# Performance work log

Hardware: AMD Instinct MI355X
Metric: run time of the kernel (lower is better)

## Reference

```python
import jax, jax.numpy as jnp
import numpy as np

S, X, G = 2048, 2048, 2
INPUT_SIZE = (3, 32, 32)
F = int(np.prod(INPUT_SIZE))


def setup_inputs() -> dict:
    key = jax.random.key(0)
    k1, k2, k3 = jax.random.split(key, 3)
    samples = jax.random.normal(k1, (S,) + INPUT_SIZE, dtype=jnp.float32)
    x = jax.random.normal(k2, (X,) + INPUT_SIZE, dtype=jnp.float32)
    # per-feature std per gradation, kept in [0.1, 1.0) like ranges_std scaling
    std = jax.random.uniform(k3, (G, F), dtype=jnp.float32, minval=0.1, maxval=1.0)
    return {"samples": samples, "x": x, "std": std}


def reference(samples, x, std):
    # samples: [S, C, H, W], x: [X, C, H, W], std: [G, F]
    G_, F_ = std.shape
    s = samples.reshape(samples.shape[0], F_)  # [S, F]
    xf = x.reshape(x.shape[0], F_)             # [X, F]
    w = 1.0 / (std * std)                       # [G, F] precision
    # per-gradation normalizer: -0.5*F*log(2pi) - sum_f log(std)
    const = -0.5 * F_ * jnp.log(2.0 * jnp.pi) - jnp.sum(jnp.log(std), axis=1)  # [G]
    # sum_f -0.5*((s-x)/std)^2 expanded: -0.5*(s^2 w - 2 s w x + x^2 w)
    A = jnp.einsum('sf,gf->gs', s * s, w)        # [G, S]
    C = jnp.einsum('xf,gf->gx', xf * xf, w)      # [G, X]
    B = jnp.einsum('sf,gf,xf->gsx', s, w, xf)    # [G, S, X] cross term
    logits = -0.5 * (A[:, :, None] - 2.0 * B + C[:, None, :]) + const[:, None, None]
    lp = jax.nn.logsumexp(logits, axis=2)        # over x (mixture components)
    lp = jax.nn.logsumexp(lp, axis=0)            # over gradations
    return lp - jnp.log(jnp.float32(x.shape[0] * G_))
```

## Files before the change

kernel.cpp:

```cpp
#include <hip/hip_runtime.h>
#include <math.h>

#define S_N 2048
#define X_N 2048
#define G_N 2
#define F_N 3072

#define TM 128
#define TN 128
#define BK 64
#define ITERS (F_N / BK)

typedef __bf16 bf16;
typedef __bf16 bf16x4 __attribute__((ext_vector_type(4)));
typedef __bf16 bf16x8 __attribute__((ext_vector_type(8)));
typedef float f32x4 __attribute__((ext_vector_type(4)));
typedef int i32x4 __attribute__((ext_vector_type(4)));

#define LGKM_BARRIER() asm volatile("s_waitcnt lgkmcnt(0)\n\ts_barrier" ::: "memory")

__global__ void k_const(const float* __restrict__ stdv, float* __restrict__ constg,
                        float* __restrict__ rinv) {
  int g = blockIdx.x;
  int t = threadIdx.x;
  float s = 0.f;
  for (int f = t; f < F_N; f += 256) {
    float v = stdv[g * F_N + f];
    rinv[g * F_N + f] = 1.0f / v;
    s += logf(v);
  }
  for (int o = 32; o; o >>= 1) s += __shfl_xor(s, o);
  __shared__ float red[4];
  int w = t >> 6, l = t & 63;
  if (l == 0) red[w] = s;
  __syncthreads();
  if (t == 0) {
    float tot = red[0] + red[1] + red[2] + red[3];
    constg[g] = -0.5f * (float)F_N * 1.8378770664093453f - tot;
  }
}

__global__ void k_prep(const float* __restrict__ samples, const float* __restrict__ xin,
                       const float* __restrict__ rinv,
                       bf16* __restrict__ U, bf16* __restrict__ V,
                       float* __restrict__ A, float* __restrict__ C) {
  int r = blockIdx.x;
  int t = threadIdx.x;
  bool isS = (r < S_N);
  const float* src = isS ? (samples + (size_t)r * F_N) : (xin + (size_t)(r - S_N) * F_N);
  float4 row[3];
#pragma unroll
  for (int j = 0; j < 3; ++j) row[j] = ((const float4*)src)[t + j * 256];

  __shared__ float red[4];
  int w = t >> 6, l = t & 63;

  for (int g = 0; g < G_N; ++g) {
    const float4* sd = (const float4*)(rinv + (size_t)g * F_N);
    bf16* dst = isS ? (U + ((size_t)g * S_N + r) * F_N)
                    : (V + ((size_t)g * X_N + (r - S_N)) * F_N);
    float acc = 0.f;
#pragma unroll
    for (int j = 0; j < 3; ++j) {
      float4 d = sd[t + j * 256];
      float u0 = row[j].x * d.x;
      float u1 = row[j].y * d.y;
      float u2 = row[j].z * d.z;
      float u3 = row[j].w * d.w;
      bf16x4 b;
      b[0] = (bf16)u0; b[1] = (bf16)u1; b[2] = (bf16)u2; b[3] = (bf16)u3;
      float f0 = (float)b[0], f1 = (float)b[1], f2 = (float)b[2], f3 = (float)b[3];
      acc += f0 * f0 + f1 * f1 + f2 * f2 + f3 * f3;
      ((bf16x4*)dst)[t + j * 256] = b;
    }
    for (int o = 32; o; o >>= 1) acc += __shfl_xor(acc, o);
    __syncthreads();
    if (l == 0) red[w] = acc;
    __syncthreads();
    if (t == 0) {
      float tot = red[0] + red[1] + red[2] + red[3];
      if (isS) A[(size_t)g * S_N + r] = tot;
      else     C[(size_t)g * X_N + (r - S_N)] = tot;
    }
  }
}

__global__ __launch_bounds__(256, 2) void k_gemm(const bf16* __restrict__ U, const bf16* __restrict__ V,
                                                 const float* __restrict__ A, const float* __restrict__ C,
                                                 float* __restrict__ logits) {
  __shared__ i32x4 ldsA[2][TM * BK / 8];
  __shared__ i32x4 ldsB[2][TN * BK / 8];

  int t = threadIdx.x;
  int g = blockIdx.z;
  int bm = blockIdx.y * TM;
  int bn = blockIdx.x * TN;

  const bf16* Ub = U + ((size_t)g * S_N + bm) * F_N;
  const bf16* Vb = V + ((size_t)g * X_N + bn) * F_N;

  int wave = t >> 6, lane = t & 63;
  int wm = wave & 1, wn = wave >> 1;
  int r = lane & 15, q = lane >> 4;
  int fr = (r >> 1) & 7;
  int ck0 = q ^ fr;
  int ck1 = (4 | q) ^ fr;

  int row0 = t >> 3;
  int gcc = (t & 7) ^ ((t >> 4) & 7);
  const bf16* gA[4];
  const bf16* gB[4];
#pragma unroll
  for (int j = 0; j < 4; ++j) {
    gA[j] = Ub + (size_t)(row0 + j * 32) * F_N + gcc * 8;
    gB[j] = Vb + (size_t)(row0 + j * 32) * F_N + gcc * 8;
  }

  f32x4 acc[4][4] = {};
  int abase = (wm * 64 + r) * 8;
  int bbase = (wn * 64 + r) * 8;

  i32x4 sA0[4], sB0[4], sA1[4], sB1[4];

#pragma unroll
  for (int j = 0; j < 4; ++j) {
    sA0[j] = *(const i32x4*)(gA[j]);
    sB0[j] = *(const i32x4*)(gB[j]);
  }
#pragma unroll
  for (int j = 0; j < 4; ++j) {
    sA1[j] = *(const i32x4*)(gA[j] + BK);
    sB1[j] = *(const i32x4*)(gB[j] + BK);
  }
#pragma unroll
  for (int j = 0; j < 4; ++j) {
    ldsA[0][t + j * 256] = sA0[j];
    ldsB[0][t + j * 256] = sB0[j];
  }
  LGKM_BARRIER();

  for (int it = 0; it < ITERS; it += 2) {
    {
      int k2 = it + 2;
      int pk = (k2 < ITERS ? k2 : 0) * BK;
#pragma unroll
      for (int j = 0; j < 4; ++j) {
        sA0[j] = *(const i32x4*)(gA[j] + pk);
        sB0[j] = *(const i32x4*)(gB[j] + pk);
      }
#pragma unroll
      for (int ks = 0; ks < 2; ++ks) {
        int ck = ks ? ck1 : ck0;
        bf16x8 af[4], bfr[4];
#pragma unroll
        for (int mi = 0; mi < 4; ++mi)
          af[mi] = __builtin_bit_cast(bf16x8, ldsA[0][abase + mi * 128 + ck]);
#pragma unroll
        for (int ni = 0; ni < 4; ++ni)
          bfr[ni] = __builtin_bit_cast(bf16x8, ldsB[0][bbase + ni * 128 + ck]);
#pragma unroll
        for (int mi = 0; mi < 4; ++mi)
#pragma unroll
          for (int ni = 0; ni < 4; ++ni)
            acc[mi][ni] = __builtin_amdgcn_mfma_f32_16x16x32_bf16(af[mi], bfr[ni], acc[mi][ni], 0, 0, 0);
      }
#pragma unroll
      for (int j = 0; j < 4; ++j) {
        ldsA[1][t + j * 256] = sA1[j];
        ldsB[1][t + j * 256] = sB1[j];
      }
      LGKM_BARRIER();
    }
    {
      int k3 = it + 3;
      int pk = (k3 < ITERS ? k3 : 0) * BK;
#pragma unroll
      for (int j = 0; j < 4; ++j) {
        sA1[j] = *(const i32x4*)(gA[j] + pk);
        sB1[j] = *(const i32x4*)(gB[j] + pk);
      }
#pragma unroll
      for (int ks = 0; ks < 2; ++ks) {
        int ck = ks ? ck1 : ck0;
        bf16x8 af[4], bfr[4];
#pragma unroll
        for (int mi = 0; mi < 4; ++mi)
          af[mi] = __builtin_bit_cast(bf16x8, ldsA[1][abase + mi * 128 + ck]);
#pragma unroll
        for (int ni = 0; ni < 4; ++ni)
          bfr[ni] = __builtin_bit_cast(bf16x8, ldsB[1][bbase + ni * 128 + ck]);
#pragma unroll
        for (int mi = 0; mi < 4; ++mi)
#pragma unroll
          for (int ni = 0; ni < 4; ++ni)
            acc[mi][ni] = __builtin_amdgcn_mfma_f32_16x16x32_bf16(af[mi], bfr[ni], acc[mi][ni], 0, 0, 0);
      }
#pragma unroll
      for (int j = 0; j < 4; ++j) {
        ldsA[0][t + j * 256] = sA0[j];
        ldsB[0][t + j * 256] = sB0[j];
      }
      LGKM_BARRIER();
    }
  }

  const float* Ap = A + (size_t)g * S_N + bm + wm * 64;
  const float* Cp = C + (size_t)g * X_N + bn + wn * 64;
  float cv[4];
#pragma unroll
  for (int ni = 0; ni < 4; ++ni) cv[ni] = Cp[ni * 16 + r];
#pragma unroll
  for (int mi = 0; mi < 4; ++mi) {
#pragma unroll
    for (int i = 0; i < 4; ++i) {
      int rowl = wm * 64 + mi * 16 + q * 4 + i;
      float av = Ap[mi * 16 + q * 4 + i];
      float* orow = logits + ((size_t)g * S_N + bm + rowl) * X_N + bn + wn * 64;
#pragma unroll
      for (int ni = 0; ni < 4; ++ni)
        orow[ni * 16 + r] = acc[mi][ni][i] - 0.5f * (av + cv[ni]);
    }
  }
}

__global__ void k_lse(const float* __restrict__ logits, const float* __restrict__ constg,
                      float* __restrict__ out) {
  int s = blockIdx.x, t = threadIdx.x;
  float c0 = constg[0], c1 = constg[1];
  const float4* p0 = (const float4*)(logits + (size_t)s * X_N);
  const float4* p1 = (const float4*)(logits + ((size_t)S_N + s) * X_N);
  float4 v[4];
  v[0] = p0[t]; v[1] = p0[t + 256];
  v[2] = p1[t]; v[3] = p1[t + 256];
  v[0].x += c0; v[0].y += c0; v[0].z += c0; v[0].w += c0;
  v[1].x += c0; v[1].y += c0; v[1].z += c0; v[1].w += c0;
  v[2].x += c1; v[2].y += c1; v[2].z += c1; v[2].w += c1;
  v[3].x += c1; v[3].y += c1; v[3].z += c1; v[3].w += c1;

  float m = v[0].x;
#pragma unroll
  for (int j = 0; j < 4; ++j) {
    m = fmaxf(m, v[j].x); m = fmaxf(m, v[j].y);
    m = fmaxf(m, v[j].z); m = fmaxf(m, v[j].w);
  }
  for (int o = 32; o; o >>= 1) m = fmaxf(m, __shfl_xor(m, o));
  __shared__ float redm[4];
  __shared__ float reds[4];
  int w = t >> 6, l = t & 63;
  if (l == 0) redm[w] = m;
  __syncthreads();
  m = fmaxf(fmaxf(redm[0], redm[1]), fmaxf(redm[2], redm[3]));

  float sum = 0.f;
#pragma unroll
  for (int j = 0; j < 4; ++j) {
    sum += expf(v[j].x - m) + expf(v[j].y - m) + expf(v[j].z - m) + expf(v[j].w - m);
  }
  for (int o = 32; o; o >>= 1) sum += __shfl_xor(sum, o);
  if (l == 0) reds[w] = sum;
  __syncthreads();
  if (t == 0) {
    float tot = reds[0] + reds[1] + reds[2] + reds[3];
    out[s] = m + logf(tot) - 8.317766166719343f;
  }
}

extern "C" void kernel_launch(void* const* d_in, const int* in_sizes, int n_in,
                              void* d_out, int out_size, void* d_ws, size_t ws_size,
                              hipStream_t stream) {
  const float* samples = (const float*)d_in[0];
  const float* xin     = (const float*)d_in[1];
  const float* stdv    = (const float*)d_in[2];
  float* out = (float*)d_out;

  char* ws = (char*)d_ws;
  size_t off = 0;
  bf16* U = (bf16*)(ws + off);        off += (size_t)G_N * S_N * F_N * 2;
  bf16* V = (bf16*)(ws + off);        off += (size_t)G_N * X_N * F_N * 2;
  float* logits = (float*)(ws + off); off += (size_t)G_N * S_N * X_N * 4;
  float* A = (float*)(ws + off);      off += (size_t)G_N * S_N * 4;
  float* C = (float*)(ws + off);      off += (size_t)G_N * X_N * 4;
  float* constg = (float*)(ws + off); off += 256;
  float* rinv = (float*)(ws + off);   off += (size_t)G_N * F_N * 4;

  k_const<<<dim3(G_N), dim3(256), 0, stream>>>(stdv, constg, rinv);
  k_prep<<<dim3(S_N + X_N), dim3(256), 0, stream>>>(samples, xin, rinv, U, V, A, C);
  k_gemm<<<dim3(X_N / TN, S_N / TM, G_N), dim3(256), 0, stream>>>(U, V, A, C, logits);
  k_lse<<<dim3(S_N), dim3(256), 0, stream>>>(logits, constg, out);
}
```

Measured before the change: 162.2 us.

## Restructure GEMM with direct global-to-LDS loads, triple buffering, and 256x128 tiles

The bf16 GEMM now loads tiles straight from global memory into LDS with global_load_lds, so the data no longer passes through registers. It also uses a three-stage LDS ring with split-phase prefetch and per-phase barriers. The block grows to 512 threads covering a 256x128 output tile. Each iteration is split into two MFMA phases with setprio and sched_barrier so loads and math interleave. This targets register pressure and global-load latency, at the cost of more LDS per block and more barriers per iteration.

```diff
diff --git a/kernel.cpp b/kernel.cpp
--- a/kernel.cpp
+++ b/kernel.cpp
@@ -1,15 +1,17 @@
 #include <hip/hip_runtime.h>
 #include <math.h>
+#include <stdint.h>
 
 #define S_N 2048
 #define X_N 2048
 #define G_N 2
 #define F_N 3072
 
-#define TM 128
+#define TM 256
 #define TN 128
 #define BK 64
 #define ITERS (F_N / BK)
+#define NBUF 3
 
 typedef __bf16 bf16;
 typedef __bf16 bf16x4 __attribute__((ext_vector_type(4)));
@@ -17,7 +19,11 @@
 typedef float f32x4 __attribute__((ext_vector_type(4)));
 typedef int i32x4 __attribute__((ext_vector_type(4)));
 
-#define LGKM_BARRIER() asm volatile("s_waitcnt lgkmcnt(0)\n\ts_barrier" ::: "memory")
+__device__ __forceinline__ void gload_lds16(const bf16* g, void* l) {
+  __builtin_amdgcn_global_load_lds(
+      (const __attribute__((address_space(1))) void*)g,
+      (__attribute__((address_space(3))) void*)l, 16, 0, 0);
+}
 
 __global__ void k_const(const float* __restrict__ stdv, float* __restrict__ constg,
                         float* __restrict__ rinv) {
@@ -85,11 +91,11 @@
   }
 }
 
-__global__ __launch_bounds__(256, 2) void k_gemm(const bf16* __restrict__ U, const bf16* __restrict__ V,
+__global__ __launch_bounds__(512, 2) void k_gemm(const bf16* __restrict__ U, const bf16* __restrict__ V,
                                                  const float* __restrict__ A, const float* __restrict__ C,
                                                  float* __restrict__ logits) {
-  __shared__ i32x4 ldsA[2][TM * BK / 8];
-  __shared__ i32x4 ldsB[2][TN * BK / 8];
+  __shared__ i32x4 ldsA[NBUF][TM * BK / 8];
+  __shared__ i32x4 ldsB[NBUF][TN * BK / 8];
 
   int t = threadIdx.x;
   int g = blockIdx.z;
@@ -100,108 +106,97 @@
   const bf16* Vb = V + ((size_t)g * X_N + bn) * F_N;
 
   int wave = t >> 6, lane = t & 63;
-  int wm = wave & 1, wn = wave >> 1;
+  int wm = wave & 3, wn = wave >> 2;
   int r = lane & 15, q = lane >> 4;
   int fr = (r >> 1) & 7;
   int ck0 = q ^ fr;
   int ck1 = (4 | q) ^ fr;
+  int abase = (wm * 64 + r) * 8;
+  int bbase = (wn * 64 + r) * 8;
 
   int row0 = t >> 3;
   int gcc = (t & 7) ^ ((t >> 4) & 7);
   const bf16* gA[4];
-  const bf16* gB[4];
-#pragma unroll
-  for (int j = 0; j < 4; ++j) {
-    gA[j] = Ub + (size_t)(row0 + j * 32) * F_N + gcc * 8;
-    gB[j] = Vb + (size_t)(row0 + j * 32) * F_N + gcc * 8;
-  }
+  const bf16* gB[2];
+#pragma unroll
+  for (int j = 0; j < 4; ++j) gA[j] = Ub + (size_t)(row0 + j * 64) * F_N + gcc * 8;
+#pragma unroll
+  for (int j = 0; j < 2; ++j) gB[j] = Vb + (size_t)(row0 + j * 64) * F_N + gcc * 8;
 
   f32x4 acc[4][4] = {};
-  int abase = (wm * 64 + r) * 8;
-  int bbase = (wn * 64 + r) * 8;
-
-  i32x4 sA0[4], sB0[4], sA1[4], sB1[4];
-
-#pragma unroll
-  for (int j = 0; j < 4; ++j) {
-    sA0[j] = *(const i32x4*)(gA[j]);
-    sB0[j] = *(const i32x4*)(gB[j]);
-  }
-#pragma unroll
-  for (int j = 0; j < 4; ++j) {
-    sA1[j] = *(const i32x4*)(gA[j] + BK);
-    sB1[j] = *(const i32x4*)(gB[j] + BK);
-  }
-#pragma unroll
-  for (int j = 0; j < 4; ++j) {
-    ldsA[0][t + j * 256] = sA0[j];
-    ldsB[0][t + j * 256] = sB0[j];
-  }
-  LGKM_BARRIER();
-
-  for (int it = 0; it < ITERS; it += 2) {
-    {
-      int k2 = it + 2;
-      int pk = (k2 < ITERS ? k2 : 0) * BK;
-#pragma unroll
-      for (int j = 0; j < 4; ++j) {
-        sA0[j] = *(const i32x4*)(gA[j] + pk);
-        sB0[j] = *(const i32x4*)(gB[j] + pk);
-      }
-#pragma unroll
-      for (int ks = 0; ks < 2; ++ks) {
-        int ck = ks ? ck1 : ck0;
-        bf16x8 af[4], bfr[4];
-#pragma unroll
-        for (int mi = 0; mi < 4; ++mi)
-          af[mi] = __builtin_bit_cast(bf16x8, ldsA[0][abase + mi * 128 + ck]);
-#pragma unroll
-        for (int ni = 0; ni < 4; ++ni)
-          bfr[ni] = __builtin_bit_cast(bf16x8, ldsB[0][bbase + ni * 128 + ck]);
-#pragma unroll
-        for (int mi = 0; mi < 4; ++mi)
-#pragma unroll
-          for (int ni = 0; ni < 4; ++ni)
-            acc[mi][ni] = __builtin_amdgcn_mfma_f32_16x16x32_bf16(af[mi], bfr[ni], acc[mi][ni], 0, 0, 0);
-      }
-#pragma unroll
-      for (int j = 0; j < 4; ++j) {
-        ldsA[1][t + j * 256] = sA1[j];
-        ldsB[1][t + j * 256] = sB1[j];
-      }
-      LGKM_BARRIER();
-    }
-    {
-      int k3 = it + 3;
-      int pk = (k3 < ITERS ? k3 : 0) * BK;
-#pragma unroll
-      for (int j = 0; j < 4; ++j) {
-        sA1[j] = *(const i32x4*)(gA[j] + pk);
-        sB1[j] = *(const i32x4*)(gB[j] + pk);
-      }
-#pragma unroll
-      for (int ks = 0; ks < 2; ++ks) {
-        int ck = ks ? ck1 : ck0;
-        bf16x8 af[4], bfr[4];
-#pragma unroll
-        for (int mi = 0; mi < 4; ++mi)
-          af[mi] = __builtin_bit_cast(bf16x8, ldsA[1][abase + mi * 128 + ck]);
-#pragma unroll
-        for (int ni = 0; ni < 4; ++ni)
-          bfr[ni] = __builtin_bit_cast(bf16x8, ldsB[1][bbase + ni * 128 + ck]);
-#pragma unroll
-        for (int mi = 0; mi < 4; ++mi)
-#pragma unroll
-          for (int ni = 0; ni < 4; ++ni)
-            acc[mi][ni] = __builtin_amdgcn_mfma_f32_16x16x32_bf16(af[mi], bfr[ni], acc[mi][ni], 0, 0, 0);
-      }
-#pragma unroll
-      for (int j = 0; j < 4; ++j) {
-        ldsA[0][t + j * 256] = sA0[j];
-        ldsB[0][t + j * 256] = sB0[j];
-      }
-      LGKM_BARRIER();
-    }
+
+#pragma unroll
+  for (int j = 0; j < 4; ++j) gload_lds16(gA[j], &ldsA[0][t + j * 512]);
+#pragma unroll
+  for (int j = 0; j < 2; ++j) gload_lds16(gB[j], &ldsB[0][t + j * 512]);
+#pragma unroll
+  for (int j = 0; j < 4; ++j) gload_lds16(gA[j] + BK, &ldsA[1][t + j * 512]);
+#pragma unroll
+  for (int j = 0; j < 2; ++j) gload_lds16(gB[j] + BK, &ldsB[1][t + j * 512]);
+  asm volatile("s_waitcnt vmcnt(6)" ::: "memory");
+  __builtin_amdgcn_s_barrier();
+
+  int cur = 0;
+  for (int it = 0; it < ITERS; ++it) {
+    int k2 = it + 2;
+    int pk = (k2 < ITERS ? k2 : 0) * BK;
+    int stg = (cur >= 1) ? cur - 1 : 2;
+    const i32x4* LA = ldsA[cur];
+    const i32x4* LB = ldsB[cur];
+
+    gload_lds16(gA[0] + pk, &ldsA[stg][t]);
+    gload_lds16(gA[1] + pk, &ldsA[stg][t + 512]);
+    gload_lds16(gA[2] + pk, &ldsA[stg][t + 1024]);
+    bf16x8 af[4][2], b01[2][2];
+#pragma unroll
+    for (int mi = 0; mi < 4; ++mi) {
+      af[mi][0] = __builtin_bit_cast(bf16x8, LA[abase + mi * 128 + ck0]);
+      af[mi][1] = __builtin_bit_cast(bf16x8, LA[abase + mi * 128 + ck1]);
+    }
+#pragma unroll
+    for (int ni = 0; ni < 2; ++ni) {
+      b01[ni][0] = __builtin_bit_cast(bf16x8, LB[bbase + ni * 128 + ck0]);
+      b01[ni][1] = __builtin_bit_cast(bf16x8, LB[bbase + ni * 128 + ck1]);
+    }
+    __builtin_amdgcn_s_barrier();
+    asm volatile("s_waitcnt lgkmcnt(0)" ::: "memory");
+    __builtin_amdgcn_sched_barrier(0);
+    __builtin_amdgcn_s_setprio(1);
+#pragma unroll
+    for (int ks = 0; ks < 2; ++ks)
+#pragma unroll
+      for (int mi = 0; mi < 4; ++mi)
+#pragma unroll
+        for (int ni = 0; ni < 2; ++ni)
+          acc[mi][ni] = __builtin_amdgcn_mfma_f32_16x16x32_bf16(af[mi][ks], b01[ni][ks], acc[mi][ni], 0, 0, 0);
+    __builtin_amdgcn_s_setprio(0);
+    __builtin_amdgcn_s_barrier();
+
+    gload_lds16(gA[3] + pk, &ldsA[stg][t + 1536]);
+    gload_lds16(gB[0] + pk, &ldsB[stg][t]);
+    gload_lds16(gB[1] + pk, &ldsB[stg][t + 512]);
+    bf16x8 b23[2][2];
+#pragma unroll
+    for (int ni = 0; ni < 2; ++ni) {
+      b23[ni][0] = __builtin_bit_cast(bf16x8, LB[bbase + (2 + ni) * 128 + ck0]);
+      b23[ni][1] = __builtin_bit_cast(bf16x8, LB[bbase + (2 + ni) * 128 + ck1]);
+    }
+    asm volatile("s_waitcnt vmcnt(6)" ::: "memory");
+    __builtin_amdgcn_s_barrier();
+    asm volatile("s_waitcnt lgkmcnt(0)" ::: "memory");
+    __builtin_amdgcn_sched_barrier(0);
+    __builtin_amdgcn_s_setprio(1);
+#pragma unroll
+    for (int ks = 0; ks < 2; ++ks)
+#pragma unroll
+      for (int mi = 0; mi < 4; ++mi)
+#pragma unroll
+        for (int ni = 0; ni < 2; ++ni)
+          acc[mi][2 + ni] = __builtin_amdgcn_mfma_f32_16x16x32_bf16(af[mi][ks], b23[ni][ks], acc[mi][2 + ni], 0, 0, 0);
+    __builtin_amdgcn_s_setprio(0);
+    __builtin_amdgcn_s_barrier();
+
+    cur = (cur == 2) ? 0 : cur + 1;
   }
 
   const float* Ap = A + (size_t)g * S_N + bm + wm * 64;
@@ -285,6 +280,6 @@
 
   k_const<<<dim3(G_N), dim3(256), 0, stream>>>(stdv, constg, rinv);
   k_prep<<<dim3(S_N + X_N), dim3(256), 0, stream>>>(samples, xin, rinv, U, V, A, C);
-  k_gemm<<<dim3(X_N / TN, S_N / TM, G_N), dim3(256), 0, stream>>>(U, V, A, C, logits);
+  k_gemm<<<dim3(X_N / TN, S_N / TM, G_N), dim3(512), 0, stream>>>(U, V, A, C, logits);
   k_lse<<<dim3(S_N), dim3(256), 0, stream>>>(logits, constg, out);
 }
```

Result: slower. 189.9 us (+17.1%).
